# Performance work log

Hardware: AMD Instinct MI355X
Metric: run time of the kernel (lower is better)

The kernel has to match this reference:

```python
import jax, jax.numpy as jnp
import numpy as np

EPS = 1e-5  # torch LayerNorm default eps

def _ln(x, g, b):
    mu = jnp.mean(x, axis=-1, keepdims=True)
    var = jnp.mean((x - mu) ** 2, axis=-1, keepdims=True)
    return (x - mu) * jax.lax.rsqrt(var + EPS) * g + b

def setup_inputs() -> dict:
    key = jax.random.key(0)
    ks = jax.random.split(key, 8)
    B, N, F, E, H = 8, 512, 64, 16, 4
    node = jax.random.normal(ks[0], (B, N, F), jnp.float32)
    edge = jax.random.normal(ks[1], (B, N, N, E), jnp.float32)
    adj = jax.random.randint(ks[2], (B, N, N), 0, 2, jnp.int32)
    s = lambda k, shp, fan: jax.random.normal(k, shp, jnp.float32) / np.sqrt(fan).astype(np.float32)
    return dict(
        node=node, edge=edge, adj=adj,
        ln1_g=jnp.ones((F,), jnp.float32), ln1_b=jnp.zeros((F,), jnp.float32),
        Wn=s(ks[3], (F, F), F), bn=jnp.zeros((F,), jnp.float32),
        ln2_g=jnp.ones((E,), jnp.float32), ln2_b=jnp.zeros((E,), jnp.float32),
        We1=s(ks[4], (2 * E, E), E), be1=jnp.zeros((2 * E,), jnp.float32),
        We2=s(ks[5], (E, 2 * E), 2 * E), be2=jnp.zeros((E,), jnp.float32),
        lne_g=jnp.ones((E,), jnp.float32), lne_b=jnp.zeros((E,), jnp.float32),
        attn_A=s(ks[6], (H, 2 * (F // H) + E), F // H),
        Wo=s(ks[7], (F, F), F), bo=jnp.zeros((F,), jnp.float32),
        lno_g=jnp.ones((F,), jnp.float32), lno_b=jnp.zeros((F,), jnp.float32),
    )

def reference(node, edge, adj, ln1_g, ln1_b, Wn, bn, ln2_g, ln2_b, We1, be1, We2, be2, lne_g, lne_b, attn_A, Wo, bo, lno_g, lno_b):
    B, N, F = node.shape
    H = attn_A.shape[0]
    hd = F // H
    node_res = node
    # node projection (dropout = identity at eval)
    h = _ln(node, ln1_g, ln1_b) @ Wn.T + bn                         # (B,N,F)
    # edge MLP with residual + layer norm
    e = _ln(edge, ln2_g, ln2_b)
    e = jax.nn.celu(e @ We1.T + be1) @ We2.T + be2
    e = _ln(e + edge, lne_g, lne_b)                                  # (B,N,N,E)
    h = h.reshape(B, N, H, hd)
    # (concat @ attn_matrix.T).sum(-1) == concat . attn_matrix.sum(0)
    a = attn_A.sum(0)                                                # (2*hd+E,)
    a_row, a_col, a_edge = a[:hd], a[hd:2 * hd], a[2 * hd:]
    sr = jnp.einsum('bnhx,x->bnh', h, a_row)                         # row term (b,i,h)
    sc = jnp.einsum('bnhx,x->bnh', h, a_col)                         # col term (b,j,h)
    se = jnp.einsum('bije,e->bij', e, a_edge)                        # edge term (b,i,j)
    logits = sr[:, :, None, :] + sc[:, None, :, :] + se[..., None]   # (B,N,N,H)
    logits = jnp.where(adj[..., None] == 0, jnp.float32(-1e9), logits)
    logits = jax.nn.leaky_relu(logits, 0.2)
    logits = jnp.clip(logits, -1e9, 1e9)
    coeffs = jax.nn.softmax(logits, axis=2)                          # softmax over j
    coeffs = jnp.nan_to_num(coeffs, nan=0.0)
    # msg[b,n,h,x] = sum_m h[b,m,h,x] * coeffs[b,n,m,h]
    msg = jnp.einsum('bmhx,bnmh->bnhx', h, coeffs).reshape(B, N, F)
    out = msg @ Wo.T + bo + node_res                                 # residual_proj == Identity (in==out)
    out = jax.nn.leaky_relu(out, 0.2)
    out = _ln(out, lno_g, lno_b)
    return (out, e, adj)
```

## Files before the change

### kernel.cpp

```cpp
#include <hip/hip_runtime.h>

#define EPS 1e-5f

__device__ __forceinline__ float wave_sum64(float v) {
    #pragma unroll
    for (int off = 32; off > 0; off >>= 1) v += __shfl_xor(v, off, 64);
    return v;
}
__device__ __forceinline__ float wave_max64(float v) {
    #pragma unroll
    for (int off = 32; off > 0; off >>= 1) v = fmaxf(v, __shfl_xor(v, off, 64));
    return v;
}

__global__ __launch_bounds__(64) void node_kernel(
    const float* __restrict__ node, const float* __restrict__ ln1_g, const float* __restrict__ ln1_b,
    const float* __restrict__ Wn, const float* __restrict__ bn, const float* __restrict__ attn_A,
    float* __restrict__ h_out, float* __restrict__ sr_out, float* __restrict__ sc_out)
{
    const int row  = blockIdx.x;
    const int lane = threadIdx.x;

    float x = node[(long)row * 64 + lane];
    float mu  = wave_sum64(x) * (1.0f / 64.0f);
    float d   = x - mu;
    float var = wave_sum64(d * d) * (1.0f / 64.0f);
    float xln = d * rsqrtf(var + EPS) * ln1_g[lane] + ln1_b[lane];

    __shared__ float xs[64];
    xs[lane] = xln;
    __syncthreads();

    float acc = bn[lane];
    const float* wrow = Wn + lane * 64;
    #pragma unroll
    for (int f = 0; f < 64; ++f) acc = fmaf(xs[f], wrow[f], acc);
    h_out[(long)row * 64 + lane] = acc;

    const int xidx = lane & 15;
    float ar = 0.f, ac = 0.f;
    #pragma unroll
    for (int hh = 0; hh < 4; ++hh) {
        ar += attn_A[hh * 48 + xidx];
        ac += attn_A[hh * 48 + 16 + xidx];
    }
    float pr = acc * ar, pc = acc * ac;
    #pragma unroll
    for (int off = 8; off > 0; off >>= 1) {
        pr += __shfl_down(pr, off, 16);
        pc += __shfl_down(pc, off, 16);
    }
    if (xidx == 0) {
        const int head = lane >> 4;
        sr_out[(long)row * 4 + head] = pr;
        sc_out[(long)row * 4 + head] = pc;
    }
}

__global__ __launch_bounds__(256, 4) void edge_kernel(
    const float* __restrict__ edge, const int* __restrict__ adj,
    const float* __restrict__ ln2_g, const float* __restrict__ ln2_b,
    const float* __restrict__ We1, const float* __restrict__ be1,
    const float* __restrict__ We2, const float* __restrict__ be2,
    const float* __restrict__ lne_g, const float* __restrict__ lne_b,
    const float* __restrict__ attn_A,
    float* __restrict__ e_out, float* __restrict__ adj_out, float* __restrict__ se_out)
{
    const long r = (long)blockIdx.x * 256 + threadIdx.x;

    const float4* ep = (const float4*)(edge + r * 16);
    float4 v0 = ep[0], v1 = ep[1], v2 = ep[2], v3 = ep[3];
    float ev[16] = { v0.x, v0.y, v0.z, v0.w, v1.x, v1.y, v1.z, v1.w,
                     v2.x, v2.y, v2.z, v2.w, v3.x, v3.y, v3.z, v3.w };

    float ae[16];
    #pragma unroll
    for (int j = 0; j < 16; ++j)
        ae[j] = attn_A[32 + j] + attn_A[48 + 32 + j] + attn_A[96 + 32 + j] + attn_A[144 + 32 + j];

    float mu = 0.f;
    #pragma unroll
    for (int i = 0; i < 16; ++i) mu += ev[i];
    mu *= (1.0f / 16.0f);
    float var = 0.f;
    #pragma unroll
    for (int i = 0; i < 16; ++i) { float d = ev[i] - mu; var += d * d; }
    var *= (1.0f / 16.0f);
    const float rs = rsqrtf(var + EPS);

    float xln[16];
    #pragma unroll
    for (int i = 0; i < 16; ++i) xln[i] = (ev[i] - mu) * rs * ln2_g[i] + ln2_b[i];

    float act[32];
    #pragma unroll
    for (int k = 0; k < 32; ++k) {
        float a = be1[k];
        #pragma unroll
        for (int i = 0; i < 16; ++i) a = fmaf(xln[i], We1[k * 16 + i], a);
        act[k] = (a > 0.f) ? a : (__expf(a) - 1.f);
    }

    float eo[16];
    #pragma unroll
    for (int j = 0; j < 16; ++j) {
        float a = be2[j];
        #pragma unroll
        for (int k = 0; k < 32; ++k) a = fmaf(act[k], We2[j * 32 + k], a);
        eo[j] = a + ev[j];
    }

    float mu2 = 0.f;
    #pragma unroll
    for (int j = 0; j < 16; ++j) mu2 += eo[j];
    mu2 *= (1.0f / 16.0f);
    float var2 = 0.f;
    #pragma unroll
    for (int j = 0; j < 16; ++j) { float d = eo[j] - mu2; var2 += d * d; }
    var2 *= (1.0f / 16.0f);
    const float rs2 = rsqrtf(var2 + EPS);

    float se = 0.f;
    #pragma unroll
    for (int j = 0; j < 16; ++j) {
        float o = (eo[j] - mu2) * rs2 * lne_g[j] + lne_b[j];
        eo[j] = o;
        se = fmaf(o, ae[j], se);
    }

    float4* op = (float4*)(e_out + r * 16);
    op[0] = make_float4(eo[0], eo[1], eo[2], eo[3]);
    op[1] = make_float4(eo[4], eo[5], eo[6], eo[7]);
    op[2] = make_float4(eo[8], eo[9], eo[10], eo[11]);
    op[3] = make_float4(eo[12], eo[13], eo[14], eo[15]);

    se_out[r]  = se;
    adj_out[r] = (float)adj[r];
}

#define G 4
__global__ __launch_bounds__(256, 4) void attn_kernel(
    const float* __restrict__ h_ws, const float* __restrict__ sr_ws, const float* __restrict__ sc_ws,
    const float* __restrict__ se_ws, const int* __restrict__ adj,
    const float* __restrict__ node, const float* __restrict__ Wo, const float* __restrict__ bo,
    const float* __restrict__ lno_g, const float* __restrict__ lno_b,
    float* __restrict__ out)
{
    const int bi0  = blockIdx.x * G;
    const int b    = bi0 >> 9;
    const int tid  = threadIdx.x;
    const int wave = tid >> 6;
    const int lane = tid & 63;

    __shared__ float coef[G][4][516];
    __shared__ float hpart[4][G][64];
    __shared__ float msg_s[G][64];

    const float4* sc4 = (const float4*)(sc_ws + (long)b * 512 * 4);

    #pragma unroll
    for (int r = 0; r < G; ++r) {
        const int row = bi0 + r;
        const float sr0 = sr_ws[(long)row * 4 + 0];
        const float sr1 = sr_ws[(long)row * 4 + 1];
        const float sr2 = sr_ws[(long)row * 4 + 2];
        const float sr3 = sr_ws[(long)row * 4 + 3];
        const float* se_row  = se_ws + (long)row * 512;
        const int*   adj_row = adj   + (long)row * 512;
        #pragma unroll
        for (int half = 0; half < 2; ++half) {
            const int j = half * 256 + tid;
            float4 s = sc4[j];
            float  se = se_row[j];
            bool   m  = (adj_row[j] != 0);
            float l0 = m ? (sr0 + s.x + se) : -1e9f;
            float l1 = m ? (sr1 + s.y + se) : -1e9f;
            float l2 = m ? (sr2 + s.z + se) : -1e9f;
            float l3 = m ? (sr3 + s.w + se) : -1e9f;
            l0 = (l0 > 0.f) ? l0 : 0.2f * l0;  l0 = fminf(fmaxf(l0, -1e9f), 1e9f);
            l1 = (l1 > 0.f) ? l1 : 0.2f * l1;  l1 = fminf(fmaxf(l1, -1e9f), 1e9f);
            l2 = (l2 > 0.f) ? l2 : 0.2f * l2;  l2 = fminf(fmaxf(l2, -1e9f), 1e9f);
            l3 = (l3 > 0.f) ? l3 : 0.2f * l3;  l3 = fminf(fmaxf(l3, -1e9f), 1e9f);
            coef[r][0][j] = l0; coef[r][1][j] = l1; coef[r][2][j] = l2; coef[r][3][j] = l3;
        }
    }
    __syncthreads();

    #pragma unroll
    for (int q = 0; q < 4; ++q) {
        const int p = q * 4 + wave;
        float* L = coef[p >> 2][p & 3];
        float v[8];
        float m = -1e30f;
        #pragma unroll
        for (int k = 0; k < 8; ++k) { v[k] = L[lane + k * 64]; m = fmaxf(m, v[k]); }
        m = wave_max64(m);
        float s = 0.f;
        #pragma unroll
        for (int k = 0; k < 8; ++k) { v[k] = __expf(v[k] - m); s += v[k]; }
        s = wave_sum64(s);
        const float inv = 1.0f / s;
        #pragma unroll
        for (int k = 0; k < 8; ++k) L[lane + k * 64] = v[k] * inv;
    }
    __syncthreads();

    {
        const int head = lane >> 4;
        const float* hb = h_ws + (long)b * 512 * 64;
        float a0 = 0.f, a1 = 0.f, a2 = 0.f, a3 = 0.f;
        const int j0 = wave * 128;
        #pragma unroll 8
        for (int j = j0; j < j0 + 128; ++j) {
            float hv = hb[(long)j * 64 + lane];
            a0 = fmaf(hv, coef[0][head][j], a0);
            a1 = fmaf(hv, coef[1][head][j], a1);
            a2 = fmaf(hv, coef[2][head][j], a2);
            a3 = fmaf(hv, coef[3][head][j], a3);
        }
        hpart[wave][0][lane] = a0;
        hpart[wave][1][lane] = a1;
        hpart[wave][2][lane] = a2;
        hpart[wave][3][lane] = a3;
    }
    __syncthreads();

    {
        const int r   = wave;
        const int row = bi0 + r;
        float m = hpart[0][r][lane] + hpart[1][r][lane] + hpart[2][r][lane] + hpart[3][r][lane];
        msg_s[r][lane] = m;

        float o = bo[lane];
        const float* wrow = Wo + lane * 64;
        #pragma unroll
        for (int ff = 0; ff < 64; ++ff) o = fmaf(msg_s[r][ff], wrow[ff], o);
        o += node[(long)row * 64 + lane];
        o = (o > 0.f) ? o : 0.2f * o;
        float mu  = wave_sum64(o) * (1.0f / 64.0f);
        float d   = o - mu;
        float var = wave_sum64(d * d) * (1.0f / 64.0f);
        out[(long)row * 64 + lane] = d * rsqrtf(var + EPS) * lno_g[lane] + lno_b[lane];
    }
}

extern "C" void kernel_launch(void* const* d_in, const int* in_sizes, int n_in,
                              void* d_out, int out_size, void* d_ws, size_t ws_size,
                              hipStream_t stream) {
    const float* node   = (const float*)d_in[0];
    const float* edge   = (const float*)d_in[1];
    const int*   adj    = (const int*)  d_in[2];
    const float* ln1_g  = (const float*)d_in[3];
    const float* ln1_b  = (const float*)d_in[4];
    const float* Wn     = (const float*)d_in[5];
    const float* bn     = (const float*)d_in[6];
    const float* ln2_g  = (const float*)d_in[7];
    const float* ln2_b  = (const float*)d_in[8];
    const float* We1    = (const float*)d_in[9];
    const float* be1    = (const float*)d_in[10];
    const float* We2    = (const float*)d_in[11];
    const float* be2    = (const float*)d_in[12];
    const float* lne_g  = (const float*)d_in[13];
    const float* lne_b  = (const float*)d_in[14];
    const float* attn_A = (const float*)d_in[15];
    const float* Wo     = (const float*)d_in[16];
    const float* bo     = (const float*)d_in[17];
    const float* lno_g  = (const float*)d_in[18];
    const float* lno_b  = (const float*)d_in[19];

    float* out_p  = (float*)d_out;
    float* e_out  = out_p + 262144;
    float* adj_o  = e_out + 33554432;

    float* ws    = (float*)d_ws;
    float* h_ws  = ws;
    float* sr_ws = ws + 262144;
    float* sc_ws = ws + 278528;
    float* se_ws = ws + 294912;

    node_kernel<<<4096, 64, 0, stream>>>(node, ln1_g, ln1_b, Wn, bn, attn_A, h_ws, sr_ws, sc_ws);
    edge_kernel<<<8192, 256, 0, stream>>>(edge, adj, ln2_g, ln2_b, We1, be1, We2, be2,
                                          lne_g, lne_b, attn_A, e_out, adj_o, se_ws);
    attn_kernel<<<1024, 256, 0, stream>>>(h_ws, sr_ws, sc_ws, se_ws, adj, node,
                                          Wo, bo, lno_g, lno_b, out_p);
}
```

Before: 344.7 us.

## Run edge MLP on bf16 MFMA with cross-lane LayerNorm reductions

Rewrites the edge kernel so each wave handles 64 edge rows in four 16-row tiles. The two small linear layers now run as bf16 16x16x32 MFMA instructions instead of per-thread scalar FMA loops, with weights packed into bf16 fragments. Each lane holds 4 features, and the LayerNorm statistics use cross-lane shuffles with a one-pass variance. This removes the large per-thread FMA count and register pressure, at the cost of bf16 rounding error in the MLP and extra shuffle traffic.

```diff
diff --git a/kernel.cpp b/kernel.cpp
--- a/kernel.cpp
+++ b/kernel.cpp
@@ -1,6 +1,11 @@
 #include <hip/hip_runtime.h>
 
 #define EPS 1e-5f
+
+typedef __attribute__((ext_vector_type(8))) short bfrag;
+typedef __attribute__((ext_vector_type(4))) float ffrag;
+
+union BFU { int i[4]; bfrag v; };
 
 __device__ __forceinline__ float wave_sum64(float v) {
     #pragma unroll
@@ -11,6 +16,18 @@
     #pragma unroll
     for (int off = 32; off > 0; off >>= 1) v = fmaxf(v, __shfl_xor(v, off, 64));
     return v;
+}
+
+__device__ __forceinline__ int pk_bf16(float a, float b) {
+    union { float f; unsigned u; } x, y;
+    x.f = a; y.f = b;
+    unsigned ra = (x.u + 0x7fffu + ((x.u >> 16) & 1u)) >> 16;
+    unsigned rb = (y.u + 0x7fffu + ((y.u >> 16) & 1u)) >> 16;
+    return (int)((rb << 16) | (ra & 0xffffu));
+}
+
+__device__ __forceinline__ float celu1(float x) {
+    return (x > 0.f) ? x : (__expf(x) - 1.f);
 }
 
 __global__ __launch_bounds__(64) void node_kernel(
@@ -66,76 +83,128 @@
     const float* __restrict__ attn_A,
     float* __restrict__ e_out, float* __restrict__ adj_out, float* __restrict__ se_out)
 {
-    const long r = (long)blockIdx.x * 256 + threadIdx.x;
-
-    const float4* ep = (const float4*)(edge + r * 16);
-    float4 v0 = ep[0], v1 = ep[1], v2 = ep[2], v3 = ep[3];
-    float ev[16] = { v0.x, v0.y, v0.z, v0.w, v1.x, v1.y, v1.z, v1.w,
-                     v2.x, v2.y, v2.z, v2.w, v3.x, v3.y, v3.z, v3.w };
-
-    float ae[16];
-    #pragma unroll
-    for (int j = 0; j < 16; ++j)
-        ae[j] = attn_A[32 + j] + attn_A[48 + 32 + j] + attn_A[96 + 32 + j] + attn_A[144 + 32 + j];
-
-    float mu = 0.f;
-    #pragma unroll
-    for (int i = 0; i < 16; ++i) mu += ev[i];
-    mu *= (1.0f / 16.0f);
-    float var = 0.f;
-    #pragma unroll
-    for (int i = 0; i < 16; ++i) { float d = ev[i] - mu; var += d * d; }
-    var *= (1.0f / 16.0f);
-    const float rs = rsqrtf(var + EPS);
-
-    float xln[16];
-    #pragma unroll
-    for (int i = 0; i < 16; ++i) xln[i] = (ev[i] - mu) * rs * ln2_g[i] + ln2_b[i];
-
-    float act[32];
-    #pragma unroll
-    for (int k = 0; k < 32; ++k) {
-        float a = be1[k];
-        #pragma unroll
-        for (int i = 0; i < 16; ++i) a = fmaf(xln[i], We1[k * 16 + i], a);
-        act[k] = (a > 0.f) ? a : (__expf(a) - 1.f);
-    }
-
-    float eo[16];
-    #pragma unroll
-    for (int j = 0; j < 16; ++j) {
-        float a = be2[j];
-        #pragma unroll
-        for (int k = 0; k < 32; ++k) a = fmaf(act[k], We2[j * 32 + k], a);
-        eo[j] = a + ev[j];
-    }
-
-    float mu2 = 0.f;
-    #pragma unroll
-    for (int j = 0; j < 16; ++j) mu2 += eo[j];
-    mu2 *= (1.0f / 16.0f);
-    float var2 = 0.f;
-    #pragma unroll
-    for (int j = 0; j < 16; ++j) { float d = eo[j] - mu2; var2 += d * d; }
-    var2 *= (1.0f / 16.0f);
-    const float rs2 = rsqrtf(var2 + EPS);
-
-    float se = 0.f;
-    #pragma unroll
-    for (int j = 0; j < 16; ++j) {
-        float o = (eo[j] - mu2) * rs2 * lne_g[j] + lne_b[j];
-        eo[j] = o;
-        se = fmaf(o, ae[j], se);
-    }
-
-    float4* op = (float4*)(e_out + r * 16);
-    op[0] = make_float4(eo[0], eo[1], eo[2], eo[3]);
-    op[1] = make_float4(eo[4], eo[5], eo[6], eo[7]);
-    op[2] = make_float4(eo[8], eo[9], eo[10], eo[11]);
-    op[3] = make_float4(eo[12], eo[13], eo[14], eo[15]);
-
-    se_out[r]  = se;
-    adj_out[r] = (float)adj[r];
+    const int tid  = threadIdx.x;
+    const int wave = tid >> 6;
+    const int lane = tid & 63;
+    const int q    = lane >> 4;
+    const int t    = lane & 15;
+    const long r0  = (long)blockIdx.x * 256 + wave * 64;
+    const int  c4  = 4 * q;
+
+    const float4 g1  = *(const float4*)(ln2_g + c4);
+    const float4 b1  = *(const float4*)(ln2_b + c4);
+    const float4 gE  = *(const float4*)(lne_g + c4);
+    const float4 bE  = *(const float4*)(lne_b + c4);
+    const float4 vb2 = *(const float4*)(be2 + c4);
+    const float4 vb1a = *(const float4*)(be1 + c4);
+    const float4 vb1b = *(const float4*)(be1 + 16 + c4);
+    float4 ae = make_float4(0.f, 0.f, 0.f, 0.f);
+    #pragma unroll
+    for (int hh = 0; hh < 4; ++hh) {
+        float4 a = *(const float4*)(attn_A + hh * 48 + 32 + c4);
+        ae.x += a.x; ae.y += a.y; ae.z += a.z; ae.w += a.w;
+    }
+
+    BFU A1[2], A2;
+    A1[0].i[0] = A1[0].i[1] = A1[0].i[2] = A1[0].i[3] = 0;
+    A1[1].i[0] = A1[1].i[1] = A1[1].i[2] = A1[1].i[3] = 0;
+    if (q < 2) {
+        #pragma unroll
+        for (int mt = 0; mt < 2; ++mt) {
+            const float* wp = We1 + (16 * mt + t) * 16 + 8 * q;
+            float4 w0 = *(const float4*)(wp);
+            float4 w1 = *(const float4*)(wp + 4);
+            A1[mt].i[0] = pk_bf16(w0.x, w0.y);
+            A1[mt].i[1] = pk_bf16(w0.z, w0.w);
+            A1[mt].i[2] = pk_bf16(w1.x, w1.y);
+            A1[mt].i[3] = pk_bf16(w1.z, w1.w);
+        }
+    }
+    {
+        const float* wp = We2 + t * 32 + 8 * q;
+        float4 w0 = *(const float4*)(wp);
+        float4 w1 = *(const float4*)(wp + 4);
+        A2.i[0] = pk_bf16(w0.x, w0.y);
+        A2.i[1] = pk_bf16(w0.z, w0.w);
+        A2.i[2] = pk_bf16(w1.x, w1.y);
+        A2.i[3] = pk_bf16(w1.z, w1.w);
+    }
+
+    const int srcA = ((q & 1) << 5) + t;
+    const int srcB = srcA + 16;
+    const bool lowhalf = (q < 2);
+
+    #pragma unroll
+    for (int nt = 0; nt < 4; ++nt) {
+        const long R = r0 + 16 * nt + t;
+        const float4 v = *(const float4*)(edge + R * 16 + c4);
+
+        float s1 = v.x + v.y + v.z + v.w;
+        float s2 = fmaf(v.x, v.x, fmaf(v.y, v.y, fmaf(v.z, v.z, v.w * v.w)));
+        s1 += __shfl_xor(s1, 16, 64); s1 += __shfl_xor(s1, 32, 64);
+        s2 += __shfl_xor(s2, 16, 64); s2 += __shfl_xor(s2, 32, 64);
+        const float mu = s1 * (1.0f / 16.0f);
+        float var = fmaxf(s2 * (1.0f / 16.0f) - mu * mu, 0.f);
+        const float rs = rsqrtf(var + EPS);
+        const float x0 = (v.x - mu) * rs * g1.x + b1.x;
+        const float x1 = (v.y - mu) * rs * g1.y + b1.y;
+        const float x2 = (v.z - mu) * rs * g1.z + b1.z;
+        const float x3 = (v.w - mu) * rs * g1.w + b1.w;
+        const int p0 = pk_bf16(x0, x1), p1 = pk_bf16(x2, x3);
+
+        BFU B1;
+        B1.i[0] = __shfl(p0, srcA, 64);
+        B1.i[1] = __shfl(p1, srcA, 64);
+        B1.i[2] = __shfl(p0, srcB, 64);
+        B1.i[3] = __shfl(p1, srcB, 64);
+
+        ffrag acc0 = { vb1a.x, vb1a.y, vb1a.z, vb1a.w };
+        ffrag acc1 = { vb1b.x, vb1b.y, vb1b.z, vb1b.w };
+        acc0 = __builtin_amdgcn_mfma_f32_16x16x32_bf16(A1[0].v, B1.v, acc0, 0, 0, 0);
+        acc1 = __builtin_amdgcn_mfma_f32_16x16x32_bf16(A1[1].v, B1.v, acc1, 0, 0, 0);
+
+        const int c0a = pk_bf16(celu1(acc0[0]), celu1(acc0[1]));
+        const int c0b = pk_bf16(celu1(acc0[2]), celu1(acc0[3]));
+        const int c1a = pk_bf16(celu1(acc1[0]), celu1(acc1[1]));
+        const int c1b = pk_bf16(celu1(acc1[2]), celu1(acc1[3]));
+
+        const int t00 = __shfl(c0a, srcA, 64), t01 = __shfl(c0b, srcA, 64);
+        const int t10 = __shfl(c1a, srcA, 64), t11 = __shfl(c1b, srcA, 64);
+        const int u00 = __shfl(c0a, srcB, 64), u01 = __shfl(c0b, srcB, 64);
+        const int u10 = __shfl(c1a, srcB, 64), u11 = __shfl(c1b, srcB, 64);
+        BFU B2;
+        B2.i[0] = lowhalf ? t00 : t10;
+        B2.i[1] = lowhalf ? t01 : t11;
+        B2.i[2] = lowhalf ? u00 : u10;
+        B2.i[3] = lowhalf ? u01 : u11;
+
+        ffrag acc2 = { vb2.x, vb2.y, vb2.z, vb2.w };
+        acc2 = __builtin_amdgcn_mfma_f32_16x16x32_bf16(A2.v, B2.v, acc2, 0, 0, 0);
+
+        const float o0 = acc2[0] + v.x;
+        const float o1 = acc2[1] + v.y;
+        const float o2 = acc2[2] + v.z;
+        const float o3 = acc2[3] + v.w;
+        float m1 = o0 + o1 + o2 + o3;
+        float m2 = fmaf(o0, o0, fmaf(o1, o1, fmaf(o2, o2, o3 * o3)));
+        m1 += __shfl_xor(m1, 16, 64); m1 += __shfl_xor(m1, 32, 64);
+        m2 += __shfl_xor(m2, 16, 64); m2 += __shfl_xor(m2, 32, 64);
+        const float mu2 = m1 * (1.0f / 16.0f);
+        float var2 = fmaxf(m2 * (1.0f / 16.0f) - mu2 * mu2, 0.f);
+        const float rs2 = rsqrtf(var2 + EPS);
+        const float e0 = (o0 - mu2) * rs2 * gE.x + bE.x;
+        const float e1 = (o1 - mu2) * rs2 * gE.y + bE.y;
+        const float e2 = (o2 - mu2) * rs2 * gE.z + bE.z;
+        const float e3 = (o3 - mu2) * rs2 * gE.w + bE.w;
+
+        *(float4*)(e_out + R * 16 + c4) = make_float4(e0, e1, e2, e3);
+
+        float sep = fmaf(e0, ae.x, fmaf(e1, ae.y, fmaf(e2, ae.z, e3 * ae.w)));
+        sep += __shfl_xor(sep, 16, 64); sep += __shfl_xor(sep, 32, 64);
+        if (q == 0) se_out[R] = sep;
+    }
+
+    adj_out[r0 + lane] = (float)adj[r0 + lane];
 }
 
 #define G 4
@@ -187,8 +256,8 @@
     __syncthreads();
 
     #pragma unroll
-    for (int q = 0; q < 4; ++q) {
-        const int p = q * 4 + wave;
+    for (int qq = 0; qq < 4; ++qq) {
+        const int p = qq * 4 + wave;
         float* L = coef[p >> 2][p & 3];
         float v[8];
         float m = -1e30f;
```

After: 329.6 us. -4.4%, faster.
